# Optimization experiments

Hardware: AMD Instinct MI355X
Metric: run time of the kernel (lower is better)

## Reference

```python
import jax, jax.numpy as jnp
import numpy as np

DELTA = 0.05
STOP = 10
INV_DELTA = 1.0 / DELTA
TOTAL = int(STOP * INV_DELTA)  # 200 bins
# slice_vol = arange(delta/2, stop, delta)**1 * delta * 2*pi*3
SLICE_VOL = (np.arange(DELTA / 2, STOP, DELTA) * DELTA * 2.0 * np.pi * 3.0).astype(np.float32)


def _cdist(a, b):
    # Euclidean pairwise distance [Na, Nb] via the (a-b)^2 = a^2 + b^2 - 2ab identity
    a2 = jnp.sum(a * a, axis=-1)
    b2 = jnp.sum(b * b, axis=-1)
    d2 = a2[:, None] + b2[None, :] - 2.0 * (a @ b.T)
    return jnp.sqrt(jnp.maximum(d2, 0.0))


def _pair_hist(pa, pb, same, real_size, vol):
    # integer distance bins; torch .int() truncates, distances are >= 0 so floor is equivalent
    bins = jnp.floor(_cdist(pa * real_size, pb * real_size) * INV_DELTA).astype(jnp.int32)
    if same:
        n = pa.shape[0]
        idx = jnp.arange(n)
        bins = bins.at[idx, idx].set(9999)  # fill_diagonal_(9999) -> excluded self-pairs
    valid = (bins < TOTAL).astype(jnp.float32).ravel()  # mask: bins beyond stop dropped
    counts = jnp.zeros(TOTAL, jnp.float32).at[jnp.clip(bins, 0, TOTAL - 1).ravel()].add(valid)
    density = pb.shape[0] / vol
    return counts / density / jnp.asarray(SLICE_VOL) / pa.shape[0]


def setup_inputs() -> dict:
    key = jax.random.key(0)
    k0, k1 = jax.random.split(key)
    pos0 = jax.random.uniform(k0, (4096, 3), dtype=jnp.float32)
    pos1 = jax.random.uniform(k1, (8192, 3), dtype=jnp.float32)
    count = jnp.zeros((2, 2, TOTAL), dtype=jnp.float32)
    real_size = jnp.array([25.0, 25.0, 3.0], dtype=jnp.float32)
    return {"pos0": pos0, "pos1": pos1, "count": count, "real_size": real_size}


def reference(pos0, pos1, count, real_size):
    vol = real_size[0] * real_size[1] * real_size[2]
    pos = [pos0, pos1]
    bufs = [
        jnp.stack([_pair_hist(pos[i], pos[j], i == j, real_size, vol) for j in range(2)])
        for i in range(2)
    ]
    # count buffer is accumulated in-place in torch; return the updated buffer
    return count + jnp.stack(bufs)
```

## Files before the change

### kernel.cpp

```cpp
#include <hip/hip_runtime.h>
#include <math.h>

#define TOTAL 200
#define TB    32
#define BLK   256
#define NW    4
#define GRID  2048
#define NR    16
#define RATIO (BLK/TB)

__global__ void rdf_prep(const float* __restrict__ p0, const float* __restrict__ p1,
                         const float* __restrict__ rs,
                         float4* __restrict__ b0, float4* __restrict__ b1,
                         unsigned int* __restrict__ ghist, int n0, int n1)
{
    const float sx = rs[0], sy = rs[1], sz = rs[2];
    int t = blockIdx.x * blockDim.x + threadIdx.x;
    if (t < n0) {
        float x = p0[t*3+0]*sx, y = p0[t*3+1]*sy, z = p0[t*3+2]*sz;
        b0[t] = make_float4(x, y, z, x*x + y*y + z*z);
    } else if (t < n0 + n1) {
        int u = t - n0;
        float x = p1[u*3+0]*sx, y = p1[u*3+1]*sy, z = p1[u*3+2]*sz;
        b1[u] = make_float4(x, y, z, x*x + y*y + z*z);
    }
    if (t < NR * 3 * TOTAL) ghist[t] = 0;
}

template<bool DIAG>
__device__ __forceinline__ void pair_loop(const float4* __restrict__ Bs,
                                          float ax, float ay, float az, float a2,
                                          unsigned int* __restrict__ mylh, int ofs)
{
    #pragma unroll 8
    for (int j = 0; j < TB; ++j) {
        float4 b  = Bs[j];
        float dot = ax*b.x + ay*b.y + az*b.z;
        float d2  = (a2 + b.w) - 2.0f*dot;
        float v   = __builtin_amdgcn_sqrtf(fmaxf(d2, 0.0f)) * 20.0f;
        bool ok   = (v < 200.0f);
        if (DIAG) ok = ok && (j > ofs);
        if (ok) atomicAdd(&mylh[(int)v], 1u);
    }
}

__global__ __launch_bounds__(BLK) void rdf_hist(
    const float4* __restrict__ b0, const float4* __restrict__ b1,
    unsigned int* __restrict__ ghist,
    int n0, int n1, int T0, int T01, int Ttot,
    int cb0, int cb1, int rows0, int rows1)
{
    __shared__ unsigned int lh[3][NW][2][TOTAL];

    const int tid  = threadIdx.x;
    const int wave = tid >> 6;
    const int par  = tid & 1;

    uint4* z = (uint4*)lh;
    for (int k = tid; k < 3*NW*2*TOTAL/4; k += BLK) z[k] = make_uint4(0,0,0,0);
    __syncthreads();

    const int gBeg = (int)(((long long)blockIdx.x       * Ttot) / GRID);
    const int gEnd = (int)(((long long)(blockIdx.x + 1) * Ttot) / GRID);

    for (int g = gBeg; g < gEnd; ++g) {
        int type, rb, cb;
        if (g < T0) {
            type = 0; rb = 0;
            while (rb + 1 < rows0 && (cb0*(rb+1) - (RATIO/2)*(rb+1)*rb) <= g) ++rb;
            cb = RATIO*rb + (g - (cb0*rb - (RATIO/2)*rb*(rb-1)));
        } else if (g < T01) {
            int u = g - T0; type = 1; rb = u / cb1; cb = u - rb*cb1;
        } else {
            int u = g - T01; type = 2; rb = 0;
            while (rb + 1 < rows1 && (cb1*(rb+1) - (RATIO/2)*(rb+1)*rb) <= u) ++rb;
            cb = RATIO*rb + (u - (cb1*rb - (RATIO/2)*rb*(rb-1)));
        }
        const float4* Ab = (type == 2) ? b1 : b0;
        const float4* Bb = (type == 0) ? b0 : b1;
        const int nA     = (type == 2) ? n1 : n0;

        const int rowBase = rb * BLK;
        const int colBase = cb * TB;
        const int aIdx    = rowBase + tid;

        float4 a = (aIdx < nA) ? Ab[aIdx]
                               : make_float4(0.f, 0.f, 0.f, 3.0e18f);
        unsigned int* mylh = &lh[type][wave][par][0];
        const float4* Bs   = Bb + colBase;

        const bool diag = (type != 1) && (colBase < rowBase + BLK);
        if (diag) pair_loop<true >(Bs, a.x, a.y, a.z, a.w, mylh, aIdx - colBase);
        else      pair_loop<false>(Bs, a.x, a.y, a.z, a.w, mylh, 0);
    }
    __syncthreads();

    unsigned int* gh = ghist + (blockIdx.x & (NR - 1)) * (3 * TOTAL);
    for (int k = tid; k < 3 * TOTAL; k += BLK) {
        int type = k / TOTAL, bin = k - type * TOTAL;
        unsigned int c = 0;
        #pragma unroll
        for (int w = 0; w < NW; ++w)
            { c += lh[type][w][0][bin] + lh[type][w][1][bin]; }
        if (c) atomicAdd(&gh[k], (type == 1) ? c : 2u * c);
    }
}

__global__ void rdf_final(const unsigned int* __restrict__ ghist,
                          const float* __restrict__ count,
                          const float* __restrict__ rs,
                          float* __restrict__ out, int n0, int n1)
{
    int t = blockIdx.x * blockDim.x + threadIdx.x;
    if (t >= 2*2*TOTAL) return;
    int k = t % TOTAL;
    int j = (t / TOTAL) & 1;
    int i = t / (2*TOTAL);

    float vol = rs[0]*rs[1]*rs[2];
    int Na = (i == 0) ? n0 : n1;
    int Nb = (j == 0) ? n0 : n1;
    int hidx = (i == j) ? (i == 0 ? 0 : 2) : 1;

    unsigned int c = 0;
    #pragma unroll
    for (int r = 0; r < NR; ++r) c += ghist[r*3*TOTAL + hidx*TOTAL + k];

    double sv  = ((0.025 + (double)k * 0.05) * 0.05) * 2.0 * M_PI * 3.0;
    float  svf = (float)sv;
    float  density = (float)Nb / vol;
    float  r = (((float)c / density) / svf) / (float)Na;
    out[t] = count[t] + r;
}

extern "C" void kernel_launch(void* const* d_in, const int* in_sizes, int n_in,
                              void* d_out, int out_size, void* d_ws, size_t ws_size,
                              hipStream_t stream) {
    const float* pos0  = (const float*)d_in[0];
    const float* pos1  = (const float*)d_in[1];
    const float* count = (const float*)d_in[2];
    const float* rs    = (const float*)d_in[3];
    float* out = (float*)d_out;

    int n0 = in_sizes[0] / 3;
    int n1 = in_sizes[1] / 3;

    unsigned int* ghist = (unsigned int*)d_ws;
    float4* b0 = (float4*)((char*)d_ws + 40960);
    float4* b1 = b0 + n0;

    int prepBlocks = (n0 + n1 + BLK - 1) / BLK;
    rdf_prep<<<prepBlocks, BLK, 0, stream>>>(pos0, pos1, rs, b0, b1, ghist, n0, n1);

    int rows0 = (n0 + BLK - 1) / BLK;
    int rows1 = (n1 + BLK - 1) / BLK;
    int cb0   = (n0 + TB - 1) / TB;
    int cb1   = (n1 + TB - 1) / TB;
    int T0   = cb0*rows0 - (RATIO/2)*rows0*(rows0-1);
    int Tc   = rows0*cb1;
    int T2   = cb1*rows1 - (RATIO/2)*rows1*(rows1-1);
    int T01  = T0 + Tc;
    int Ttot = T01 + T2;

    rdf_hist<<<GRID, BLK, 0, stream>>>(b0, b1, ghist, n0, n1,
                                       T0, T01, Ttot, cb0, cb1, rows0, rows1);

    rdf_final<<<(2*2*TOTAL + BLK - 1) / BLK, BLK, 0, stream>>>(ghist, count, rs, out, n0, n1);
}
```

Before: 103.1 us.

## Double-buffer B tile in shared memory with next-tile prefetch

Each block now stages the 32-point B tile into a double-buffered shared array, with one wave prefetching the next tile's points while all threads process the current tile from LDS. Before, every thread read B points straight from global memory, relying on cache broadcast. The change adds a block-wide barrier per tile and extra tile decoding by the loading threads, trading global/L1 reads for LDS reads and synchronisation.

```diff
diff --git a/kernel.cpp b/kernel.cpp
--- a/kernel.cpp
+++ b/kernel.cpp
@@ -27,6 +27,26 @@
     if (t < NR * 3 * TOTAL) ghist[t] = 0;
 }
 
+struct Tile { int type, rb, cb; };
+
+__device__ __forceinline__ Tile decode(int g, int T0, int T01,
+                                       int cb0, int cb1, int rows0, int rows1)
+{
+    Tile t;
+    if (g < T0) {
+        t.type = 0; t.rb = 0;
+        while (t.rb + 1 < rows0 && (cb0*(t.rb+1) - (RATIO/2)*(t.rb+1)*t.rb) <= g) ++t.rb;
+        t.cb = RATIO*t.rb + (g - (cb0*t.rb - (RATIO/2)*t.rb*(t.rb-1)));
+    } else if (g < T01) {
+        int u = g - T0; t.type = 1; t.rb = u / cb1; t.cb = u - t.rb*cb1;
+    } else {
+        int u = g - T01; t.type = 2; t.rb = 0;
+        while (t.rb + 1 < rows1 && (cb1*(t.rb+1) - (RATIO/2)*(t.rb+1)*t.rb) <= u) ++t.rb;
+        t.cb = RATIO*t.rb + (u - (cb1*t.rb - (RATIO/2)*t.rb*(t.rb-1)));
+    }
+    return t;
+}
+
 template<bool DIAG>
 __device__ __forceinline__ void pair_loop(const float4* __restrict__ Bs,
                                           float ax, float ay, float az, float a2,
@@ -51,6 +71,7 @@
     int cb0, int cb1, int rows0, int rows1)
 {
     __shared__ unsigned int lh[3][NW][2][TOTAL];
+    __shared__ float4 Bst[2][TB];
 
     const int tid  = threadIdx.x;
     const int wave = tid >> 6;
@@ -58,38 +79,40 @@
 
     uint4* z = (uint4*)lh;
     for (int k = tid; k < 3*NW*2*TOTAL/4; k += BLK) z[k] = make_uint4(0,0,0,0);
-    __syncthreads();
 
     const int gBeg = (int)(((long long)blockIdx.x       * Ttot) / GRID);
     const int gEnd = (int)(((long long)(blockIdx.x + 1) * Ttot) / GRID);
 
+    if (tid < TB) {
+        Tile t0 = decode(gBeg, T0, T01, cb0, cb1, rows0, rows1);
+        const float4* Bb = (t0.type == 0) ? b0 : b1;
+        Bst[0][tid] = Bb[t0.cb * TB + tid];
+    }
+
     for (int g = gBeg; g < gEnd; ++g) {
-        int type, rb, cb;
-        if (g < T0) {
-            type = 0; rb = 0;
-            while (rb + 1 < rows0 && (cb0*(rb+1) - (RATIO/2)*(rb+1)*rb) <= g) ++rb;
-            cb = RATIO*rb + (g - (cb0*rb - (RATIO/2)*rb*(rb-1)));
-        } else if (g < T01) {
-            int u = g - T0; type = 1; rb = u / cb1; cb = u - rb*cb1;
-        } else {
-            int u = g - T01; type = 2; rb = 0;
-            while (rb + 1 < rows1 && (cb1*(rb+1) - (RATIO/2)*(rb+1)*rb) <= u) ++rb;
-            cb = RATIO*rb + (u - (cb1*rb - (RATIO/2)*rb*(rb-1)));
+        __syncthreads();
+        const int p = (g - gBeg) & 1;
+
+        if (tid < TB && g + 1 < gEnd) {
+            Tile tn = decode(g + 1, T0, T01, cb0, cb1, rows0, rows1);
+            const float4* Bb = (tn.type == 0) ? b0 : b1;
+            Bst[p ^ 1][tid] = Bb[tn.cb * TB + tid];
         }
-        const float4* Ab = (type == 2) ? b1 : b0;
-        const float4* Bb = (type == 0) ? b0 : b1;
-        const int nA     = (type == 2) ? n1 : n0;
 
-        const int rowBase = rb * BLK;
-        const int colBase = cb * TB;
+        Tile t = decode(g, T0, T01, cb0, cb1, rows0, rows1);
+        const float4* Ab = (t.type == 2) ? b1 : b0;
+        const int nA     = (t.type == 2) ? n1 : n0;
+
+        const int rowBase = t.rb * BLK;
+        const int colBase = t.cb * TB;
         const int aIdx    = rowBase + tid;
 
         float4 a = (aIdx < nA) ? Ab[aIdx]
                                : make_float4(0.f, 0.f, 0.f, 3.0e18f);
-        unsigned int* mylh = &lh[type][wave][par][0];
-        const float4* Bs   = Bb + colBase;
+        unsigned int* mylh = &lh[t.type][wave][par][0];
+        const float4* Bs   = &Bst[p][0];
 
-        const bool diag = (type != 1) && (colBase < rowBase + BLK);
+        const bool diag = (t.type != 1) && (colBase < rowBase + BLK);
         if (diag) pair_loop<true >(Bs, a.x, a.y, a.z, a.w, mylh, aIdx - colBase);
         else      pair_loop<false>(Bs, a.x, a.y, a.z, a.w, mylh, 0);
     }
```

Result: no change. 104.7 us (+1.5%).
